# Kernel tuning notes

Hardware: AMD Instinct MI355X
Metric: run time of the kernel (lower is better)

Reference implementation:

```python
import jax, jax.numpy as jnp
import numpy as np

N_WIRES = 4
N_LAYERS = 3
BATCH = 65536
BN_EPS = 1e-5


def setup_inputs() -> dict:
    key = jax.random.key(0)
    k = jax.random.split(key, 4)
    return {
        "x": jax.random.normal(k[0], (BATCH, 1, 28, 28), dtype=jnp.float32),
        "params": jax.random.normal(k[1], (N_LAYERS, N_WIRES, 3), dtype=jnp.float32),
        "W": jax.random.normal(k[2], (4, N_WIRES), dtype=jnp.float32) * 0.5,
        "b": jax.random.normal(k[3], (4,), dtype=jnp.float32) * 0.1,
        "bn_weight": jnp.ones((4,), dtype=jnp.float32),
        "bn_bias": jnp.zeros((4,), dtype=jnp.float32),
    }


def _fused_rzrx(params):
    """Precompute M[l,w] = RX(params[l,w,1]) @ RZ(params[l,w,0]); shape (L,W,2,2) complex.
    (params[...,2] is unused by the original circuit.)"""
    t0 = params[..., 0]
    t1 = params[..., 1]
    ez = jnp.exp(-0.5j * t0)          # RZ diag entries: (ez, conj(ez))
    ezc = jnp.exp(0.5j * t0)
    cx = jnp.cos(0.5 * t1) + 0j
    sx = -1j * jnp.sin(0.5 * t1)
    row0 = jnp.stack([cx * ez, sx * ezc], axis=-1)
    row1 = jnp.stack([sx * ez, cx * ezc], axis=-1)
    return jnp.stack([row0, row1], axis=-2).astype(jnp.complex64)


def _ry(t):
    c = jnp.cos(0.5 * t) + 0j
    s = jnp.sin(0.5 * t) + 0j
    return jnp.stack([jnp.stack([c, -s]), jnp.stack([s, c])]).astype(jnp.complex64)


def _sim_one(xv, M):
    """Statevector simulation of the 4-wire variational circuit for one sample.
    xv: (4,) encoding angles; M: (L,W,2,2) fused RX@RZ gates. Returns (4,) PauliZ expvals."""
    state = jnp.zeros((2,) * N_WIRES, dtype=jnp.complex64).at[0, 0, 0, 0].set(1.0)
    rys = [_ry(xv[w]) for w in range(N_WIRES)]
    for i in range(N_LAYERS):
        for w in range(N_WIRES):
            U = M[i, w] @ rys[w]  # RY then RZ then RX, fused into one 2x2
            state = jnp.moveaxis(jnp.tensordot(U, state, axes=([1], [w])), 0, w)
            if w < N_WIRES - 1:
                # CNOT(control=w, target=w+1): flip target amps where control=1
                s = jnp.moveaxis(state, (w, w + 1), (0, 1))
                s = s.at[1].set(s[1, ::-1])
                state = jnp.moveaxis(s, (0, 1), (w, w + 1))
    probs = jnp.real(state * jnp.conj(state))  # (2,2,2,2)
    zs = []
    for w in range(N_WIRES):
        other = tuple(a for a in range(N_WIRES) if a != w)
        m = probs.sum(axis=other)  # marginal over wire w
        zs.append(m[0] - m[1])
    return jnp.stack(zs)


def reference(x, params, W, b, bn_weight, bn_bias):
    bsz = x.shape[0]
    flat = x.reshape(bsz, -1)
    # chunk into 4 equal groups and mean each -> (B, 4) encoding angles
    enc = flat.reshape(bsz, N_WIRES, -1).mean(axis=-1)
    M = _fused_rzrx(params)
    z = jax.vmap(_sim_one, in_axes=(0, None))(enc, M).astype(jnp.float32)  # (B, 4)
    out = z @ W.T + b  # Linear(4, 4)
    # BatchNorm1d (training mode, biased variance)
    mu = out.mean(axis=0)
    var = ((out - mu) ** 2).mean(axis=0)
    return (out - mu) * jax.lax.rsqrt(var + BN_EPS) * bn_weight + bn_bias
```

## Files before the change

kernel.cpp:

```cpp
#include <hip/hip_runtime.h>

#define BATCH 65536
#define BN_EPS 1e-5f

__global__ __launch_bounds__(64) void gates_kernel(const float* __restrict__ params,
                                                   float* __restrict__ Mbuf) {
    int t = threadIdx.x;
    if (t < 12) {
        float t0 = params[t * 3 + 0];
        float t1 = params[t * 3 + 1];
        float s0 = sinf(0.5f * t0), c0 = cosf(0.5f * t0);
        float s1 = sinf(0.5f * t1), c1 = cosf(0.5f * t1);
        float* m = Mbuf + t * 8;
        m[0] = c1 * c0;   m[1] = -c1 * s0;
        m[2] = s1 * s0;   m[3] = -s1 * c0;
        m[4] = -s1 * s0;  m[5] = -s1 * c0;
        m[6] = c1 * c0;   m[7] = c1 * s0;
    }
}

__global__ __launch_bounds__(256) void encode_kernel(const float* __restrict__ x,
                                                     float* __restrict__ enc,
                                                     int batch) {
    int wave = (int)((blockIdx.x * blockDim.x + threadIdx.x) >> 6);
    int lane = threadIdx.x & 63;
    if (wave >= batch) return;
    const float4* xs = (const float4*)(x + (size_t)wave * 784);
    float s0 = 0.f, s1 = 0.f, s2 = 0.f, s3 = 0.f;
#pragma unroll
    for (int it = 0; it < 4; it++) {
        int f = it * 64 + lane;
        if (f < 196) {
            float4 v = xs[f];
            float vs = v.x + v.y + v.z + v.w;
            int g = f / 49;
            s0 += (g == 0) ? vs : 0.0f;
            s1 += (g == 1) ? vs : 0.0f;
            s2 += (g == 2) ? vs : 0.0f;
            s3 += (g == 3) ? vs : 0.0f;
        }
    }
#pragma unroll
    for (int off = 32; off > 0; off >>= 1) {
        s0 += __shfl_down(s0, off);
        s1 += __shfl_down(s1, off);
        s2 += __shfl_down(s2, off);
        s3 += __shfl_down(s3, off);
    }
    if (lane == 0) {
        const float inv = 1.0f / 196.0f;
        ((float4*)enc)[wave] = make_float4(s0 * inv, s1 * inv, s2 * inv, s3 * inv);
    }
}

__global__ __launch_bounds__(256) void sim_kernel(const float* __restrict__ enc,
                                                  const float* __restrict__ Mbuf,
                                                  const float* __restrict__ Wm,
                                                  const float* __restrict__ bvec,
                                                  float* __restrict__ out_ws,
                                                  float* __restrict__ sums) {
    int t = blockIdx.x * blockDim.x + threadIdx.x;
    float4 e = ((const float4*)enc)[t];
    float ang[4] = {e.x, e.y, e.z, e.w};
    float cw[4], sw[4];
#pragma unroll
    for (int w = 0; w < 4; w++) {
        __sincosf(0.5f * ang[w], &sw[w], &cw[w]);
    }

    float sr[16], si[16];
#pragma unroll
    for (int i = 0; i < 16; i++) { sr[i] = 0.f; si[i] = 0.f; }
    sr[0] = 1.0f;

#pragma unroll
    for (int l = 0; l < 3; l++) {
#pragma unroll
        for (int w = 0; w < 4; w++) {
            const float* m = Mbuf + (l * 4 + w) * 8;
            float c = cw[w], s = sw[w];
            float u00r = m[0] * c + m[2] * s;
            float u00i = m[1] * c + m[3] * s;
            float u01r = -m[0] * s + m[2] * c;
            float u01i = -m[1] * s + m[3] * c;
            float u10r = m[4] * c + m[6] * s;
            float u10i = m[5] * c + m[7] * s;
            float u11r = -m[4] * s + m[6] * c;
            float u11i = -m[5] * s + m[7] * c;
            const int stride = 8 >> w;
#pragma unroll
            for (int i = 0; i < 16; i++) {
                if (i & stride) continue;
                int j = i | stride;
                float a0r = sr[i], a0i = si[i];
                float a1r = sr[j], a1i = si[j];
                sr[i] = u00r * a0r - u00i * a0i + u01r * a1r - u01i * a1i;
                si[i] = u00r * a0i + u00i * a0r + u01r * a1i + u01i * a1r;
                sr[j] = u10r * a0r - u10i * a0i + u11r * a1r - u11i * a1i;
                si[j] = u10r * a0i + u10i * a0r + u11r * a1i + u11i * a1r;
            }
            if (w < 3) {
                const int ts = 8 >> (w + 1);
#pragma unroll
                for (int i = 0; i < 16; i++) {
                    if (!(i & stride)) continue;
                    if (i & ts) continue;
                    int j = i | ts;
                    float tr = sr[i]; sr[i] = sr[j]; sr[j] = tr;
                    float ti = si[i]; si[i] = si[j]; si[j] = ti;
                }
            }
        }
    }

    float p[16];
#pragma unroll
    for (int i = 0; i < 16; i++) p[i] = sr[i] * sr[i] + si[i] * si[i];
    float z[4];
#pragma unroll
    for (int w = 0; w < 4; w++) {
        const int stride = 8 >> w;
        float acc = 0.f;
#pragma unroll
        for (int i = 0; i < 16; i++) acc += (i & stride) ? -p[i] : p[i];
        z[w] = acc;
    }

    float o[4];
#pragma unroll
    for (int j = 0; j < 4; j++) {
        o[j] = bvec[j] + Wm[j * 4 + 0] * z[0] + Wm[j * 4 + 1] * z[1] +
               Wm[j * 4 + 2] * z[2] + Wm[j * 4 + 3] * z[3];
    }
    ((float4*)out_ws)[t] = make_float4(o[0], o[1], o[2], o[3]);

    float vals[8];
#pragma unroll
    for (int j = 0; j < 4; j++) { vals[j] = o[j]; vals[4 + j] = o[j] * o[j]; }
#pragma unroll
    for (int k = 0; k < 8; k++) {
#pragma unroll
        for (int off = 32; off > 0; off >>= 1) vals[k] += __shfl_down(vals[k], off);
    }
    __shared__ float part[4][8];
    int lane = threadIdx.x & 63;
    int wv = threadIdx.x >> 6;
    if (lane == 0) {
#pragma unroll
        for (int k = 0; k < 8; k++) part[wv][k] = vals[k];
    }
    __syncthreads();
    if (threadIdx.x == 0) {
#pragma unroll
        for (int k = 0; k < 8; k++) {
            float tsum = part[0][k] + part[1][k] + part[2][k] + part[3][k];
            atomicAdd(&sums[k], tsum);
        }
    }
}

__global__ __launch_bounds__(64) void bn_finalize_kernel(const float* __restrict__ sums,
                                                         const float* __restrict__ bn_w,
                                                         const float* __restrict__ bn_b,
                                                         float* __restrict__ scsh,
                                                         float inv_batch) {
    int j = threadIdx.x;
    if (j < 4) {
        float mu = sums[j] * inv_batch;
        float ex2 = sums[4 + j] * inv_batch;
        float var = ex2 - mu * mu;
        float sc = bn_w[j] * rsqrtf(var + BN_EPS);
        scsh[j] = sc;
        scsh[4 + j] = bn_b[j] - mu * sc;
    }
}

__global__ __launch_bounds__(256) void norm_kernel(const float* __restrict__ out_ws,
                                                   const float* __restrict__ scsh,
                                                   float* __restrict__ dout) {
    int t = blockIdx.x * blockDim.x + threadIdx.x;
    float4 o = ((const float4*)out_ws)[t];
    float4 sc = ((const float4*)scsh)[0];
    float4 sh = ((const float4*)scsh)[1];
    ((float4*)dout)[t] = make_float4(o.x * sc.x + sh.x, o.y * sc.y + sh.y,
                                     o.z * sc.z + sh.z, o.w * sc.w + sh.w);
}

extern "C" void kernel_launch(void* const* d_in, const int* in_sizes, int n_in,
                              void* d_out, int out_size, void* d_ws, size_t ws_size,
                              hipStream_t stream) {
    const float* x      = (const float*)d_in[0];
    const float* params = (const float*)d_in[1];
    const float* Wm     = (const float*)d_in[2];
    const float* bvec   = (const float*)d_in[3];
    const float* bn_w   = (const float*)d_in[4];
    const float* bn_b   = (const float*)d_in[5];
    float* dout = (float*)d_out;

    const int B = in_sizes[0] / 784;

    float* ws   = (float*)d_ws;
    float* Mbuf = ws;
    float* sums = ws + 96;
    float* scsh = ws + 104;
    float* enc  = ws + 128;
    float* outw = ws + 128 + 4 * (size_t)B;

    gates_kernel<<<1, 64, 0, stream>>>(params, Mbuf);
    hipMemsetAsync(sums, 0, 8 * sizeof(float), stream);
    encode_kernel<<<(B + 3) / 4, 256, 0, stream>>>(x, enc, B);
    sim_kernel<<<B / 256, 256, 0, stream>>>(enc, Mbuf, Wm, bvec, outw, sums);
    bn_finalize_kernel<<<1, 64, 0, stream>>>(sums, bn_w, bn_b, scsh, 1.0f / (float)B);
    norm_kernel<<<B / 256, 256, 0, stream>>>(outw, scsh, dout);
}
```

Baseline: 320.9 us.

## Fold gate and BN-finalize kernels into consumers; straighten encode loads

Removes the separate gates kernel by computing the fused RX·RZ gate matrices per block in shared memory inside the sim kernel. It also folds the batch-norm finalize into the norm kernel, where each block recomputes scale and shift. Together this cuts two launches and their serialization gaps. The encode kernel now issues four unconditional float4 loads with lane-range masks instead of a loop with a per-element divide. The cost is redundant per-block trig and a block barrier, and encode drops the batch bound check, so it assumes the batch is a multiple of 4.

```diff
diff --git a/kernel.cpp b/kernel.cpp
--- a/kernel.cpp
+++ b/kernel.cpp
@@ -1,45 +1,28 @@
 #include <hip/hip_runtime.h>
 
-#define BATCH 65536
 #define BN_EPS 1e-5f
 
-__global__ __launch_bounds__(64) void gates_kernel(const float* __restrict__ params,
-                                                   float* __restrict__ Mbuf) {
-    int t = threadIdx.x;
-    if (t < 12) {
-        float t0 = params[t * 3 + 0];
-        float t1 = params[t * 3 + 1];
-        float s0 = sinf(0.5f * t0), c0 = cosf(0.5f * t0);
-        float s1 = sinf(0.5f * t1), c1 = cosf(0.5f * t1);
-        float* m = Mbuf + t * 8;
-        m[0] = c1 * c0;   m[1] = -c1 * s0;
-        m[2] = s1 * s0;   m[3] = -s1 * c0;
-        m[4] = -s1 * s0;  m[5] = -s1 * c0;
-        m[6] = c1 * c0;   m[7] = c1 * s0;
-    }
-}
-
 __global__ __launch_bounds__(256) void encode_kernel(const float* __restrict__ x,
-                                                     float* __restrict__ enc,
-                                                     int batch) {
+                                                     float* __restrict__ enc) {
     int wave = (int)((blockIdx.x * blockDim.x + threadIdx.x) >> 6);
     int lane = threadIdx.x & 63;
-    if (wave >= batch) return;
     const float4* xs = (const float4*)(x + (size_t)wave * 784);
-    float s0 = 0.f, s1 = 0.f, s2 = 0.f, s3 = 0.f;
-#pragma unroll
-    for (int it = 0; it < 4; it++) {
-        int f = it * 64 + lane;
-        if (f < 196) {
-            float4 v = xs[f];
-            float vs = v.x + v.y + v.z + v.w;
-            int g = f / 49;
-            s0 += (g == 0) ? vs : 0.0f;
-            s1 += (g == 1) ? vs : 0.0f;
-            s2 += (g == 2) ? vs : 0.0f;
-            s3 += (g == 3) ? vs : 0.0f;
-        }
-    }
+
+    float4 v0 = xs[lane];
+    float4 v1 = xs[64 + lane];
+    float4 v2 = xs[128 + lane];
+    float4 v3 = (lane < 4) ? xs[192 + lane] : make_float4(0.f, 0.f, 0.f, 0.f);
+
+    float t0 = (v0.x + v0.y) + (v0.z + v0.w);
+    float t1 = (v1.x + v1.y) + (v1.z + v1.w);
+    float t2 = (v2.x + v2.y) + (v2.z + v2.w);
+    float t3 = (v3.x + v3.y) + (v3.z + v3.w);
+
+    float s0 = (lane < 49) ? t0 : 0.f;
+    float s1 = ((lane >= 49) ? t0 : 0.f) + ((lane < 34) ? t1 : 0.f);
+    float s2 = ((lane >= 34) ? t1 : 0.f) + ((lane < 19) ? t2 : 0.f);
+    float s3 = ((lane >= 19) ? t2 : 0.f) + t3;
+
 #pragma unroll
     for (int off = 32; off > 0; off >>= 1) {
         s0 += __shfl_down(s0, off);
@@ -54,19 +37,38 @@
 }
 
 __global__ __launch_bounds__(256) void sim_kernel(const float* __restrict__ enc,
-                                                  const float* __restrict__ Mbuf,
+                                                  const float* __restrict__ params,
                                                   const float* __restrict__ Wm,
                                                   const float* __restrict__ bvec,
                                                   float* __restrict__ out_ws,
                                                   float* __restrict__ sums) {
+    __shared__ float G[96];
+    __shared__ float WB[20];
+    if (threadIdx.x < 12) {
+        int t = threadIdx.x;
+        float t0 = params[t * 3 + 0];
+        float t1 = params[t * 3 + 1];
+        float s0, c0, s1, c1;
+        __sincosf(0.5f * t0, &s0, &c0);
+        __sincosf(0.5f * t1, &s1, &c1);
+        float* m = G + t * 8;
+        m[0] = c1 * c0;   m[1] = -c1 * s0;
+        m[2] = s1 * s0;   m[3] = -s1 * c0;
+        m[4] = -s1 * s0;  m[5] = -s1 * c0;
+        m[6] = c1 * c0;   m[7] = c1 * s0;
+    } else if (threadIdx.x < 32) {
+        int k = threadIdx.x - 12;
+        if (k < 16) WB[k] = Wm[k];
+        else WB[k] = bvec[k - 16];
+    }
+    __syncthreads();
+
     int t = blockIdx.x * blockDim.x + threadIdx.x;
     float4 e = ((const float4*)enc)[t];
     float ang[4] = {e.x, e.y, e.z, e.w};
     float cw[4], sw[4];
 #pragma unroll
-    for (int w = 0; w < 4; w++) {
-        __sincosf(0.5f * ang[w], &sw[w], &cw[w]);
-    }
+    for (int w = 0; w < 4; w++) __sincosf(0.5f * ang[w], &sw[w], &cw[w]);
 
     float sr[16], si[16];
 #pragma unroll
@@ -77,7 +79,7 @@
     for (int l = 0; l < 3; l++) {
 #pragma unroll
         for (int w = 0; w < 4; w++) {
-            const float* m = Mbuf + (l * 4 + w) * 8;
+            const float* m = G + (l * 4 + w) * 8;
             float c = cw[w], s = sw[w];
             float u00r = m[0] * c + m[2] * s;
             float u00i = m[1] * c + m[3] * s;
@@ -129,8 +131,8 @@
     float o[4];
 #pragma unroll
     for (int j = 0; j < 4; j++) {
-        o[j] = bvec[j] + Wm[j * 4 + 0] * z[0] + Wm[j * 4 + 1] * z[1] +
-               Wm[j * 4 + 2] * z[2] + Wm[j * 4 + 3] * z[3];
+        o[j] = WB[16 + j] + WB[j * 4 + 0] * z[0] + WB[j * 4 + 1] * z[1] +
+               WB[j * 4 + 2] * z[2] + WB[j * 4 + 3] * z[3];
     }
     ((float4*)out_ws)[t] = make_float4(o[0], o[1], o[2], o[3]);
 
@@ -159,31 +161,27 @@
     }
 }
 
-__global__ __launch_bounds__(64) void bn_finalize_kernel(const float* __restrict__ sums,
-                                                         const float* __restrict__ bn_w,
-                                                         const float* __restrict__ bn_b,
-                                                         float* __restrict__ scsh,
-                                                         float inv_batch) {
-    int j = threadIdx.x;
-    if (j < 4) {
+__global__ __launch_bounds__(256) void norm_kernel(const float* __restrict__ out_ws,
+                                                   const float* __restrict__ sums,
+                                                   const float* __restrict__ bn_w,
+                                                   const float* __restrict__ bn_b,
+                                                   float* __restrict__ dout,
+                                                   float inv_batch) {
+    __shared__ float sc[4], sh[4];
+    if (threadIdx.x < 4) {
+        int j = threadIdx.x;
         float mu = sums[j] * inv_batch;
         float ex2 = sums[4 + j] * inv_batch;
         float var = ex2 - mu * mu;
-        float sc = bn_w[j] * rsqrtf(var + BN_EPS);
-        scsh[j] = sc;
-        scsh[4 + j] = bn_b[j] - mu * sc;
-    }
-}
-
-__global__ __launch_bounds__(256) void norm_kernel(const float* __restrict__ out_ws,
-                                                   const float* __restrict__ scsh,
-                                                   float* __restrict__ dout) {
+        float s = bn_w[j] * rsqrtf(var + BN_EPS);
+        sc[j] = s;
+        sh[j] = bn_b[j] - mu * s;
+    }
+    __syncthreads();
     int t = blockIdx.x * blockDim.x + threadIdx.x;
     float4 o = ((const float4*)out_ws)[t];
-    float4 sc = ((const float4*)scsh)[0];
-    float4 sh = ((const float4*)scsh)[1];
-    ((float4*)dout)[t] = make_float4(o.x * sc.x + sh.x, o.y * sc.y + sh.y,
-                                     o.z * sc.z + sh.z, o.w * sc.w + sh.w);
+    ((float4*)dout)[t] = make_float4(o.x * sc[0] + sh[0], o.y * sc[1] + sh[1],
+                                     o.z * sc[2] + sh[2], o.w * sc[3] + sh[3]);
 }
 
 extern "C" void kernel_launch(void* const* d_in, const int* in_sizes, int n_in,
@@ -200,16 +198,12 @@
     const int B = in_sizes[0] / 784;
 
     float* ws   = (float*)d_ws;
-    float* Mbuf = ws;
-    float* sums = ws + 96;
-    float* scsh = ws + 104;
-    float* enc  = ws + 128;
-    float* outw = ws + 128 + 4 * (size_t)B;
-
-    gates_kernel<<<1, 64, 0, stream>>>(params, Mbuf);
+    float* sums = ws;
+    float* enc  = ws + 64;
+    float* outw = ws + 64 + 4 * (size_t)B;
+
     hipMemsetAsync(sums, 0, 8 * sizeof(float), stream);
-    encode_kernel<<<(B + 3) / 4, 256, 0, stream>>>(x, enc, B);
-    sim_kernel<<<B / 256, 256, 0, stream>>>(enc, Mbuf, Wm, bvec, outw, sums);
-    bn_finalize_kernel<<<1, 64, 0, stream>>>(sums, bn_w, bn_b, scsh, 1.0f / (float)B);
-    norm_kernel<<<B / 256, 256, 0, stream>>>(outw, scsh, dout);
-}
+    encode_kernel<<<B / 4, 256, 0, stream>>>(x, enc);
+    sim_kernel<<<B / 256, 256, 0, stream>>>(enc, params, Wm, bvec, outw, sums);
+    norm_kernel<<<B / 256, 256, 0, stream>>>(outw, sums, bn_w, bn_b, dout, 1.0f / (float)B);
+}
```

Result: no change. 319.1 us (-0.5%).
